# Performance work log

Hardware: AMD Instinct MI355X
Metric: run time of the kernel (lower is better)

The kernel has to match this reference:

```python
import jax, jax.numpy as jnp
import numpy as np

B, N, H_DIM = 64, 128, 128
NODE_S, NODE_V = 64, 32            # irreps_node = 64x0e + 32x1o -> dim 160
OUT_S, OUT_V = 32, 16              # out irreps  = 32x0e + 16x1o -> dim 80
RBF, ZEMB, HID, LAT, EDIM, NE = 16, 32, 128, 256, 16, 512
EATT = 4096
CUTOFF = 5.0
MAXZ = 100
NODE_DIM = NODE_S + 3 * NODE_V
OUT_DIM = OUT_S + 3 * OUT_V
WN = NODE_S*OUT_S + NODE_V*OUT_S + NODE_S*OUT_V + NODE_V*OUT_V  # 4608 TP weights per edge
GATE_IN = H_DIM + H_DIM + RBF + 1

def _lin(k, fi, fo):
    return jax.random.normal(k, (fi, fo), jnp.float32) / np.sqrt(fi)

def setup_inputs() -> dict:
    ks = jax.random.split(jax.random.key(0), 24)
    flat = B * N
    att_dist = jax.random.uniform(ks[0], (EATT,), jnp.float32, 0.05, CUTOFF)
    dirs = jax.random.normal(ks[1], (EATT, 3), jnp.float32)
    dirs = dirs / jnp.linalg.norm(dirs, axis=-1, keepdims=True)
    return dict(
        h=jax.random.normal(ks[2], (B, N, H_DIM), jnp.float32),
        h_full=jax.random.normal(ks[3], (B, N, NODE_DIM), jnp.float32),
        z=jax.random.randint(ks[4], (B, N), 1, MAXZ + 1),
        mask=jnp.ones((B, N), bool),
        e_feat=jax.random.normal(ks[5], (NE, EDIM), jnp.float32),
        absorber_index=jax.random.randint(ks[6], (B,), 0, N),
        att_dst=jax.random.randint(ks[7], (EATT,), 0, flat),
        att_dist=att_dist,
        att_vec=dirs * att_dist[:, None],
        w_zemb=jax.random.normal(ks[8], (MAXZ + 1, ZEMB), jnp.float32),
        w1_rad=_lin(ks[9], ZEMB + 1 + RBF, HID), b1_rad=jnp.zeros(HID, jnp.float32),
        w2_rad=_lin(ks[10], HID, WN), b2_rad=jnp.zeros(WN, jnp.float32),
        wg1=_lin(ks[11], GATE_IN, HID), bg1=jnp.zeros(HID, jnp.float32),
        wg2=_lin(ks[12], HID, 1), bg2=jnp.zeros(1, jnp.float32),
        we1=_lin(ks[13], EDIM, HID), be1=jnp.zeros(HID, jnp.float32),
        we2=_lin(ks[14], HID, OUT_S + OUT_V), be2=jnp.ones(OUT_S + OUT_V, jnp.float32),
        wo1=_lin(ks[15], OUT_S + OUT_V, HID), bo1=jnp.zeros(HID, jnp.float32),
        wo2=_lin(ks[16], HID, HID), bo2=jnp.zeros(HID, jnp.float32),
        wo3=_lin(ks[17], HID, LAT), bo3=jnp.zeros(LAT, jnp.float32),
    )

def _core(h, h_full, z, e_feat, absorber_index, att_dst, att_dist, att_vec,
          w_zemb, w1_rad, b1_rad, w2_rad, b2_rad, wg1, bg1, wg2, bg2,
          we1, be1, we2, be2, wo1, bo1, wo2, bo2, wo3, bo3):
    B_, N_, H_ = h.shape
    flat = B_ * N_
    dt = h.dtype
    # scatter edge data into flat (B*N) buffers
    amask = jnp.zeros((flat,), bool).at[att_dst].set(True)
    dflat = jnp.zeros((flat,), dt).at[att_dst].set(att_dist.astype(dt))
    vflat = jnp.zeros((flat, 3), dt).at[att_dst].set(att_vec.astype(dt))
    eps = jnp.maximum(dflat, 1e-8)
    u = vflat / eps[:, None]
    # component-normalized real spherical harmonics, lmax=1: Y0 = 1, Y1 = sqrt(3)*u
    ys = jnp.ones((flat, 1), dt)
    yv = jnp.sqrt(jnp.asarray(3.0, dt)) * u
    # Gaussian RBF on distance
    centers = jnp.linspace(0.0, CUTOFF, RBF).astype(dt)
    width = CUTOFF / (RBF - 1)
    rbf = jnp.exp(-0.5 * ((dflat[:, None] - centers) / width) ** 2)
    zr = w_zemb[z].reshape(flat, ZEMB)
    is_abs = jax.nn.one_hot(absorber_index, N_, dtype=dt)  # (B,N)
    win = jnp.concatenate([zr, is_abs.reshape(flat, 1), rbf], -1)
    tpw = jax.nn.silu(win @ w1_rad + b1_rad) @ w2_rad + b2_rad  # (flat, WN)
    o = 0
    wA = tpw[:, o:o + NODE_S*OUT_S].reshape(flat, NODE_S, OUT_S); o += NODE_S*OUT_S
    wB = tpw[:, o:o + NODE_V*OUT_S].reshape(flat, NODE_V, OUT_S); o += NODE_V*OUT_S
    wC = tpw[:, o:o + NODE_S*OUT_V].reshape(flat, NODE_S, OUT_V); o += NODE_S*OUT_V
    wD = tpw[:, o:o + NODE_V*OUT_V].reshape(flat, NODE_V, OUT_V)
    hf = h_full.reshape(flat, NODE_DIM)
    s1 = hf[:, :NODE_S]
    v1 = hf[:, NODE_S:].reshape(flat, NODE_V, 3)
    norm = 1.0 / np.sqrt(NODE_S + NODE_V)   # TP path (fan-in) normalization
    inv_s3 = 1.0 / np.sqrt(3.0)             # CG(1,1->0) = delta/sqrt(3)
    out_s = (jnp.einsum('ei,eio->eo', s1 * ys, wA)
             + jnp.einsum('eic,ec,eio->eo', v1, yv, wB) * inv_s3) * norm
    out_v = (jnp.einsum('ei,eio->eo', s1, wC)[:, :, None] * yv[:, None, :]
             + jnp.einsum('eic,eio->eoc', v1, wD) * ys[:, :, None]) * norm
    ve = jnp.concatenate([out_s, out_v.reshape(flat, 3 * OUT_V)], -1)
    env = jnp.where(dflat < CUTOFF, 0.5 * (jnp.cos(np.pi * dflat / CUTOFF) + 1.0), 0.0)[:, None]
    ve = ve * env
    # PaiNN-style scalar edge gate
    h_abs = jnp.take_along_axis(h, absorber_index[:, None, None], axis=1)  # (B,1,H)
    gate_in = jnp.concatenate([jnp.broadcast_to(h_abs, (B_, N_, H_)), h,
                               rbf.reshape(B_, N_, RBF), is_abs[..., None]], -1)
    gate = jax.nn.sigmoid(jax.nn.silu(gate_in @ wg1 + bg1) @ wg2 + bg2).reshape(flat, 1)
    ve = ve * gate * amask[:, None].astype(dt)
    v_abs = ve.reshape(B_, N_, OUT_DIM).sum(1)  # (B, OUT_DIM)
    # energy irrep modulation: per-mul scalar from energy features
    scales = jax.nn.silu(e_feat @ we1 + be1) @ we2 + be2  # (nE, OUT_S+OUT_V)
    scale_full = jnp.concatenate([scales[:, :OUT_S], jnp.repeat(scales[:, OUT_S:], 3, axis=-1)], -1)
    v_mod = v_abs[:, None, :] * scale_full[None]  # (B, nE, OUT_DIM)
    vecs = v_mod[..., OUT_S:].reshape(B_, scales.shape[0], OUT_V, 3)
    inv = jnp.concatenate([v_mod[..., :OUT_S], jnp.sqrt(jnp.sum(vecs * vecs, -1) + 1e-12)], -1)
    x = jax.nn.silu(inv @ wo1 + bo1)
    x = jax.nn.silu(x @ wo2 + bo2)
    return x @ wo3 + bo3  # (B, nE, LAT)

def reference(h, h_full, z, mask, e_feat, absorber_index, att_dst, att_dist, att_vec,
              w_zemb, w1_rad, b1_rad, w2_rad, b2_rad, wg1, bg1, wg2, bg2,
              we1, be1, we2, be2, wo1, bo1, wo2, bo2, wo3, bo3):
    # mask is computed into att_mask in the original but never used downstream
    return _core(h, h_full, z, e_feat, absorber_index, att_dst, att_dist, att_vec,
                 w_zemb, w1_rad, b1_rad, w2_rad, b2_rad, wg1, bg1, wg2, bg2,
                 we1, be1, we2, be2, wo1, bo1, wo2, bo2, wo3, bo3)
```

## Files before the change

### kernel.cpp

```cpp
#include <hip/hip_runtime.h>
#include <math.h>

#define FLAT   8192
#define NB     64
#define OD_    80
#define NE_    512
#define EATT_  4096
#define MAXACT 4096
#define PARTW 1088

typedef __bf16 v8bf __attribute__((ext_vector_type(8)));
typedef float  v4f  __attribute__((ext_vector_type(4)));

__device__ __forceinline__ float silu_f(float x) { return x / (1.f + __expf(-x)); }
__device__ __forceinline__ float sigm_f(float x) { return 1.f / (1.f + __expf(-x)); }

__device__ __forceinline__ void transpose_split(const float* __restrict__ src, int ld,
                                                int nbase, __bf16* wh, __bf16* wl,
                                                float (*lds)[129]) {
  int t = threadIdx.x;
#pragma unroll
  for (int it = 0; it < 16; ++it) {
    int idx = it * 256 + t;
    int r = idx >> 5, c4 = idx & 31;
    float4 v = *(const float4*)(src + (size_t)r * ld + nbase + c4 * 4);
    lds[r][c4 * 4 + 0] = v.x;
    lds[r][c4 * 4 + 1] = v.y;
    lds[r][c4 * 4 + 2] = v.z;
    lds[r][c4 * 4 + 3] = v.w;
  }
  __syncthreads();
  int n = t >> 1, kh = (t & 1) * 64;
  union { __bf16 b[64]; uint4 u[8]; } H, L;
#pragma unroll
  for (int k = 0; k < 64; ++k) {
    float v = lds[kh + k][n];
    __bf16 hv = (__bf16)v;
    H.b[k] = hv;
    L.b[k] = (__bf16)(v - (float)hv);
  }
  uint4* ph = (uint4*)(wh + (size_t)(nbase + n) * 128 + kh);
  uint4* pl = (uint4*)(wl + (size_t)(nbase + n) * 128 + kh);
#pragma unroll
  for (int i = 0; i < 8; ++i) { ph[i] = H.u[i]; pl[i] = L.u[i]; }
}

__global__ __launch_bounds__(256) void k_prep(
    const float* __restrict__ w2_rad, const float* __restrict__ wo2,
    const float* __restrict__ wo3,
    const int* __restrict__ abs_idx, const float* __restrict__ h,
    const float* __restrict__ wg1,
    __bf16* w2rt_h, __bf16* w2rt_l, __bf16* w2t_h, __bf16* w2t_l,
    __bf16* w3t_h, __bf16* w3t_l,
    float* habs_g, float* vabs, int* widx, int* count) {
  __shared__ float lds[128][129];
  int bid = blockIdx.x;
  int t = threadIdx.x;
  if (bid < 36) {
    transpose_split(w2_rad, 4608, bid * 128, w2rt_h, w2rt_l, lds);
  } else if (bid < 37) {
    transpose_split(wo2, 128, 0, w2t_h, w2t_l, lds);
  } else if (bid < 39) {
    transpose_split(wo3, 256, (bid - 37) * 128, w3t_h, w3t_l, lds);
  } else if (bid < 71) {
    float* hs = &lds[0][0];
    int half = t >> 7, tt = t & 127;
    int b = (bid - 39) * 2 + half;
    int nabs = abs_idx[b];
    hs[half * 128 + tt] = h[(size_t)(b * 128 + nabs) * 128 + tt];
    __syncthreads();
    float g = 0.f;
    for (int c = 0; c < 128; ++c) g = fmaf(hs[half * 128 + c], wg1[c * 128 + tt], g);
    habs_g[b * 128 + tt] = g;
  } else {
    int g = (bid - 71) * 256 + t;
    if (g < FLAT) widx[g] = -1;
    if (g < NB * OD_) vabs[g] = 0.f;
    if (g == 0) *count = 0;
  }
}

__global__ void k_scatter(const int* __restrict__ att_dst, int* widx) {
  int i = blockIdx.x * 256 + threadIdx.x;
  if (i < EATT_) atomicMax(&widx[att_dst[i]], i);
}

__global__ void k_build(const int* __restrict__ widx, int* active, int* count) {
  int j = blockIdx.x * 256 + threadIdx.x;
  if (j < FLAT && widx[j] >= 0) {
    int p = atomicAdd(count, 1);
    active[p] = j;
  }
}

__global__ __launch_bounds__(128) void k_node4(
    const int* __restrict__ count, const int* __restrict__ active,
    const int* __restrict__ widx,
    const float* __restrict__ att_dist, const float* __restrict__ att_vec,
    const int* __restrict__ z, const float* __restrict__ w_zemb,
    const int* __restrict__ abs_idx,
    const float* __restrict__ w1_rad, const float* __restrict__ b1_rad,
    const float* __restrict__ h, const float* __restrict__ habs_g,
    const float* __restrict__ wg1, const float* __restrict__ bg1,
    const float* __restrict__ wg2, const float* __restrict__ bg2,
    const float* __restrict__ h_full,
    __bf16* ah_glob, __bf16* al_glob,
    float* coef_glob, float* meta_f, int* meta_b) {
  int cnt = *count;
  int pbase = blockIdx.x * 4;
  if (pbase >= cnt) return;
  int t = threadIdx.x;

  __shared__ float win[4][49];
  __shared__ float yv_s[4][3];
  __shared__ float sh_d[4];
  __shared__ float red[4][128];
  __shared__ float hsh[4][128];

  bool ok[4];
  int jj[4], ee[4], bb[4];
  float isab[4];
#pragma unroll
  for (int q = 0; q < 4; ++q) {
    int pos = pbase + q;
    ok[q] = pos < cnt;
    jj[q] = ok[q] ? active[pos] : 0;
    ee[q] = ok[q] ? widx[jj[q]] : 0;
    if (ee[q] < 0) ee[q] = 0;
    bb[q] = jj[q] >> 7;
    isab[q] = ((jj[q] & 127) == abs_idx[bb[q]]) ? 1.f : 0.f;
  }

  if (t < 4) {
    int q = t;
    float d = att_dist[ee[q]];
    sh_d[q] = d;
    float eps = fmaxf(d, 1e-8f);
    const float s3 = 1.7320508075688772f;
    yv_s[q][0] = s3 * att_vec[ee[q] * 3 + 0] / eps;
    yv_s[q][1] = s3 * att_vec[ee[q] * 3 + 1] / eps;
    yv_s[q][2] = s3 * att_vec[ee[q] * 3 + 2] / eps;
  }
#pragma unroll
  for (int q = 0; q < 4; ++q) {
    if (t < 32) win[q][t] = w_zemb[z[jj[q]] * 32 + t];
    if (t == 32) win[q][32] = isab[q];
    if (t >= 33 && t < 49) {
      int k = t - 33;
      float d = att_dist[ee[q]];
      float x = (d - (float)k * (1.f / 3.f)) * 3.f;
      win[q][t] = __expf(-0.5f * x * x);
    }
    hsh[q][t] = h[(size_t)jj[q] * 128 + t];
  }
  __syncthreads();

  {
    float s[4];
    float bv = b1_rad[t];
#pragma unroll
    for (int q = 0; q < 4; ++q) s[q] = bv;
    for (int k = 0; k < 49; ++k) {
      float wv = w1_rad[k * 128 + t];
#pragma unroll
      for (int q = 0; q < 4; ++q) s[q] = fmaf(win[q][k], wv, s[q]);
    }
#pragma unroll
    for (int q = 0; q < 4; ++q) {
      if (ok[q]) {
        float av = silu_f(s[q]);
        __bf16 hv = (__bf16)av;
        ah_glob[(size_t)(pbase + q) * 128 + t] = hv;
        al_glob[(size_t)(pbase + q) * 128 + t] = (__bf16)(av - (float)hv);
      }
    }
  }

  {
    float g[4];
#pragma unroll
    for (int q = 0; q < 4; ++q) g[q] = bg1[t] + habs_g[bb[q] * 128 + t];
    for (int c = 0; c < 128; ++c) {
      float wv = wg1[(128 + c) * 128 + t];
#pragma unroll
      for (int q = 0; q < 4; ++q) g[q] = fmaf(hsh[q][c], wv, g[q]);
    }
    for (int k = 0; k < 16; ++k) {
      float wv = wg1[(256 + k) * 128 + t];
#pragma unroll
      for (int q = 0; q < 4; ++q) g[q] = fmaf(win[q][33 + k], wv, g[q]);
    }
    {
      float wv = wg1[272 * 128 + t];
#pragma unroll
      for (int q = 0; q < 4; ++q) g[q] = fmaf(isab[q], wv, g[q]);
    }
    float w2v = wg2[t];
#pragma unroll
    for (int q = 0; q < 4; ++q) red[q][t] = silu_f(g[q]) * w2v;
  }
  __syncthreads();

#pragma unroll
  for (int q = 0; q < 4; ++q) {
    if (!ok[q]) continue;
    int pos = pbase + q;
    const float* hf = h_full + (size_t)jj[q] * 160;
    if (t < 64) coef_glob[pos * 192 + t] = hf[t];
    if (t >= 64 && t < 96) {
      int i = t - 64;
      float pv = hf[64 + i * 3 + 0] * yv_s[q][0] + hf[64 + i * 3 + 1] * yv_s[q][1] +
                 hf[64 + i * 3 + 2] * yv_s[q][2];
      coef_glob[pos * 192 + t] = pv * 0.5773502691896258f;
    }
    if (t < 96) coef_glob[pos * 192 + 96 + t] = hf[64 + t];
  }

  if (t < 4) {
    int q = t;
    if (ok[q]) {
      int pos = pbase + q;
      float tot = 0.f;
      for (int k = 0; k < 128; ++k) tot += red[q][k];
      tot += bg2[0];
      float gate = sigm_f(tot);
      float d = sh_d[q];
      float env = (d < 5.f) ? 0.5f * (__cosf(3.14159265358979323846f * d * 0.2f) + 1.f) : 0.f;
      meta_f[pos * 4 + 0] = yv_s[q][0];
      meta_f[pos * 4 + 1] = yv_s[q][1];
      meta_f[pos * 4 + 2] = yv_s[q][2];
      meta_f[pos * 4 + 3] = gate * env;
      meta_b[pos] = bb[q];
    }
  }
}

__global__ __launch_bounds__(256) void k_mrgemm(
    const int* __restrict__ count,
    const __bf16* Ah, const __bf16* Al,
    const __bf16* __restrict__ Bh, const __bf16* __restrict__ Bl,
    const float* __restrict__ b2, const float* __restrict__ coef_glob,
    float* __restrict__ part) {
  int cc = blockIdx.x;
  int nbase = blockIdx.y * 128;
  int cnt = *count;
  if (nbase >= cnt) return;
  int t = threadIdx.x;
  int w = t >> 6, l = t & 63;
  int kg = l >> 4, ln = l & 15;
  int cbase = cc * 128;

  __shared__ v8bf Bs[2][2][8][64];

  size_t brow0 = (size_t)(cbase + w * 16 + ln) * 128 + kg * 8;
  size_t brow1 = (size_t)(cbase + (w + 4) * 16 + ln) * 128 + kg * 8;
  size_t arow0 = (size_t)(nbase + (2 * w) * 16 + ln) * 128 + kg * 8;
  size_t arow1 = (size_t)(nbase + (2 * w + 1) * 16 + ln) * 128 + kg * 8;

  v8bf rb0 = *(const v8bf*)(Bh + brow0);
  v8bf rb1 = *(const v8bf*)(Bh + brow1);
  v8bf rb2 = *(const v8bf*)(Bl + brow0);
  v8bf rb3 = *(const v8bf*)(Bl + brow1);
  v8bf ah0 = *(const v8bf*)(Ah + arow0);
  v8bf al0 = *(const v8bf*)(Al + arow0);
  v8bf ah1 = *(const v8bf*)(Ah + arow1);
  v8bf al1 = *(const v8bf*)(Al + arow1);
  Bs[0][0][w][l]     = rb0;
  Bs[0][0][w + 4][l] = rb1;
  Bs[0][1][w][l]     = rb2;
  Bs[0][1][w + 4][l] = rb3;
  __syncthreads();

  v4f acc[2][8];
  v4f z4 = {0.f, 0.f, 0.f, 0.f};
#pragma unroll
  for (int i = 0; i < 2; ++i)
#pragma unroll
    for (int j = 0; j < 8; ++j) acc[i][j] = z4;

  for (int kb = 0; kb < 4; ++kb) {
    int cur = kb & 1;
    v8bf nb0, nb1, nb2, nb3, nh0, nl0, nh1, nl1;
    if (kb < 3) {
      int off = (kb + 1) * 32;
      nb0 = *(const v8bf*)(Bh + brow0 + off);
      nb1 = *(const v8bf*)(Bh + brow1 + off);
      nb2 = *(const v8bf*)(Bl + brow0 + off);
      nb3 = *(const v8bf*)(Bl + brow1 + off);
      nh0 = *(const v8bf*)(Ah + arow0 + off);
      nl0 = *(const v8bf*)(Al + arow0 + off);
      nh1 = *(const v8bf*)(Ah + arow1 + off);
      nl1 = *(const v8bf*)(Al + arow1 + off);
    }
#pragma unroll
    for (int nt = 0; nt < 8; ++nt) {
      v8bf bh = Bs[cur][0][nt][l];
      v8bf bl = Bs[cur][1][nt][l];
      acc[0][nt] = __builtin_amdgcn_mfma_f32_16x16x32_bf16(ah0, bh, acc[0][nt], 0, 0, 0);
      acc[0][nt] = __builtin_amdgcn_mfma_f32_16x16x32_bf16(al0, bh, acc[0][nt], 0, 0, 0);
      acc[0][nt] = __builtin_amdgcn_mfma_f32_16x16x32_bf16(ah0, bl, acc[0][nt], 0, 0, 0);
      acc[1][nt] = __builtin_amdgcn_mfma_f32_16x16x32_bf16(ah1, bh, acc[1][nt], 0, 0, 0);
      acc[1][nt] = __builtin_amdgcn_mfma_f32_16x16x32_bf16(al1, bh, acc[1][nt], 0, 0, 0);
      acc[1][nt] = __builtin_amdgcn_mfma_f32_16x16x32_bf16(ah1, bl, acc[1][nt], 0, 0, 0);
    }
    if (kb < 3) {
      int nxt = cur ^ 1;
      Bs[nxt][0][w][l]     = nb0;
      Bs[nxt][0][w + 4][l] = nb1;
      Bs[nxt][1][w][l]     = nb2;
      Bs[nxt][1][w + 4][l] = nb3;
      ah0 = nh0; al0 = nl0; ah1 = nh1; al1 = nl1;
    }
    __syncthreads();
  }

  float b2v[8];
#pragma unroll
  for (int nt = 0; nt < 8; ++nt) b2v[nt] = b2[cbase + nt * 16 + ln];

#pragma unroll
  for (int mi = 0; mi < 2; ++mi) {
    int nodeb = nbase + (2 * w + mi) * 16 + kg * 4;
#pragma unroll
    for (int j = 0; j < 4; ++j) {
      int nd = nodeb + j;
      if (nd >= cnt) continue;
      const float* cf = coef_glob + (size_t)nd * 192;
      if (cc < 24) {
        float s0 = 0.f, s1 = 0.f;
#pragma unroll
        for (int m = 0; m < 4; ++m) {
          float c = cf[cc * 4 + m];
          s0 = fmaf(acc[mi][2 * m][j] + b2v[2 * m], c, s0);
          s1 = fmaf(acc[mi][2 * m + 1][j] + b2v[2 * m + 1], c, s1);
        }
        float* pp = part + (size_t)nd * PARTW + cc * 32 + ln;
        pp[0]  = s0;
        pp[16] = s1;
      } else if (cc < 32) {
        float s = 0.f;
#pragma unroll
        for (int nt = 0; nt < 8; ++nt)
          s = fmaf(acc[mi][nt][j] + b2v[nt], cf[(cc - 24) * 8 + nt], s);
        part[(size_t)nd * PARTW + 768 + (cc - 24) * 16 + ln] = s;
      } else {
        float s0 = 0.f, s1 = 0.f, s2 = 0.f;
#pragma unroll
        for (int nt = 0; nt < 8; ++nt) {
          float x = acc[mi][nt][j] + b2v[nt];
          const float* c3 = cf + 96 + ((cc - 32) * 8 + nt) * 3;
          s0 = fmaf(x, c3[0], s0);
          s1 = fmaf(x, c3[1], s1);
          s2 = fmaf(x, c3[2], s2);
        }
        float* pp = part + (size_t)nd * PARTW + 896 + (cc - 32) * 48 + ln;
        pp[0]  = s0;
        pp[16] = s1;
        pp[32] = s2;
      }
    }
  }
}

__global__ __launch_bounds__(256) void k_post(
    const int* __restrict__ count, const float* __restrict__ part,
    const float* __restrict__ meta_f, const int* __restrict__ meta_b, float* vabs,
    const float* __restrict__ e_feat,
    const float* __restrict__ we1, const float* __restrict__ be1,
    const float* __restrict__ we2, const float* __restrict__ be2, float* sfull) {
  __shared__ float hid[128];
  int t = threadIdx.x;
  if (blockIdx.x < 2048) {
    int pos = blockIdx.x * 2 + (t >> 7);
    int slot = t & 127;
    if (pos >= *count || slot >= 96) return;
    const float* pp = part + (size_t)pos * PARTW;
    float s = 0.f;
    if (slot < 32) {
#pragma unroll
      for (int c = 0; c < 24; ++c) s += pp[c * 32 + slot];
    } else if (slot < 48) {
#pragma unroll
      for (int c = 0; c < 8; ++c) s += pp[768 + c * 16 + (slot - 32)];
    } else {
#pragma unroll
      for (int c = 0; c < 4; ++c) s += pp[896 + c * 48 + (slot - 48)];
    }
    float sc = meta_f[pos * 4 + 3] * 0.10206207261596577f;
    float* vb = vabs + meta_b[pos] * 80;
    if (slot < 32) {
      unsafeAtomicAdd(&vb[slot], s * sc);
    } else if (slot < 48) {
      int o = slot - 32;
      float q = s * sc;
      unsafeAtomicAdd(&vb[32 + o * 3 + 0], q * meta_f[pos * 4 + 0]);
      unsafeAtomicAdd(&vb[32 + o * 3 + 1], q * meta_f[pos * 4 + 1]);
      unsafeAtomicAdd(&vb[32 + o * 3 + 2], q * meta_f[pos * 4 + 2]);
    } else {
      int s2 = slot - 48;
      int comp = s2 >> 4, o = s2 & 15;
      unsafeAtomicAdd(&vb[32 + o * 3 + comp], s * sc);
    }
  } else {
    int row = blockIdx.x - 2048;
    if (t < 128) {
      const float* ef = e_feat + row * 16;
      float s = be1[t];
      for (int k = 0; k < 16; ++k) s = fmaf(ef[k], we1[k * 128 + t], s);
      hid[t] = silu_f(s);
    }
    __syncthreads();
    if (t < 48) {
      float o = be2[t];
      for (int k = 0; k < 128; ++k) o = fmaf(hid[k], we2[k * 48 + t], o);
      if (t < 32) sfull[row * 80 + t] = o;
      else {
        int oo = t - 32;
        sfull[row * 80 + 32 + oo * 3 + 0] = o;
        sfull[row * 80 + 32 + oo * 3 + 1] = o;
        sfull[row * 80 + 32 + oo * 3 + 2] = o;
      }
    }
  }
}

__global__ __launch_bounds__(256) void k_hg1(const float* __restrict__ vabs,
                                             const float* __restrict__ sfull,
                                             const float* __restrict__ wo1,
                                             const float* __restrict__ bo1,
                                             __bf16* __restrict__ xh,
                                             __bf16* __restrict__ xl) {
  int rbase = blockIdx.x * 64;
  int b = rbase >> 9;
  int e0 = rbase & 511;
  int t = threadIdx.x;
  int tx = t & 15, ty = t >> 4;
  int n0 = ty * 4;

  __shared__ float w_s[48 * 128];
  __shared__ float invt[48][64];
  __shared__ float va[80];

  if (t < 80) va[t] = vabs[b * 80 + t];
  {
    const float4* wg = (const float4*)wo1;
    float4* ws4 = (float4*)w_s;
#pragma unroll
    for (int it = 0; it < 6; ++it) ws4[t + it * 256] = wg[t + it * 256];
  }
  __syncthreads();

  for (int idx = t; idx < 48 * 64; idx += 256) {
    int cd = idx >> 6, r = idx & 63;
    const float* sf = sfull + (size_t)(e0 + r) * 80;
    float v;
    if (cd < 32) v = va[cd] * sf[cd];
    else {
      int base = 32 + (cd - 32) * 3;
      float m0 = va[base + 0] * sf[base + 0];
      float m1 = va[base + 1] * sf[base + 1];
      float m2 = va[base + 2] * sf[base + 2];
      v = sqrtf(m0 * m0 + m1 * m1 + m2 * m2 + 1e-12f);
    }
    invt[cd][r] = v;
  }
  __syncthreads();

  float acc[4][8];
#pragma unroll
  for (int i = 0; i < 4; ++i)
#pragma unroll
    for (int j = 0; j < 8; ++j) acc[i][j] = 0.f;

  for (int k = 0; k < 48; ++k) {
    float4 av  = *(const float4*)&invt[k][n0];
    float4 w0  = *(const float4*)&w_s[k * 128 + tx * 4];
    float4 w1v = *(const float4*)&w_s[k * 128 + 64 + tx * 4];
#pragma unroll
    for (int i = 0; i < 4; ++i) {
      float a = (i == 0) ? av.x : (i == 1) ? av.y : (i == 2) ? av.z : av.w;
      acc[i][0] = fmaf(a, w0.x,  acc[i][0]);
      acc[i][1] = fmaf(a, w0.y,  acc[i][1]);
      acc[i][2] = fmaf(a, w0.z,  acc[i][2]);
      acc[i][3] = fmaf(a, w0.w,  acc[i][3]);
      acc[i][4] = fmaf(a, w1v.x, acc[i][4]);
      acc[i][5] = fmaf(a, w1v.y, acc[i][5]);
      acc[i][6] = fmaf(a, w1v.z, acc[i][6]);
      acc[i][7] = fmaf(a, w1v.w, acc[i][7]);
    }
  }

  float4 bq0 = *(const float4*)(bo1 + tx * 4);
  float4 bq1 = *(const float4*)(bo1 + 64 + tx * 4);
#pragma unroll
  for (int i = 0; i < 4; ++i) {
    size_t row = (size_t)(rbase + n0 + i);
    float q0[4] = {silu_f(acc[i][0] + bq0.x), silu_f(acc[i][1] + bq0.y),
                   silu_f(acc[i][2] + bq0.z), silu_f(acc[i][3] + bq0.w)};
    float q1[4] = {silu_f(acc[i][4] + bq1.x), silu_f(acc[i][5] + bq1.y),
                   silu_f(acc[i][6] + bq1.z), silu_f(acc[i][7] + bq1.w)};
    union { __bf16 bb[4]; uint2 u; } H, L;
#pragma unroll
    for (int e = 0; e < 4; ++e) {
      __bf16 hv = (__bf16)q0[e];
      H.bb[e] = hv;
      L.bb[e] = (__bf16)(q0[e] - (float)hv);
    }
    *(uint2*)(xh + row * 128 + tx * 4) = H.u;
    *(uint2*)(xl + row * 128 + tx * 4) = L.u;
#pragma unroll
    for (int e = 0; e < 4; ++e) {
      __bf16 hv = (__bf16)q1[e];
      H.bb[e] = hv;
      L.bb[e] = (__bf16)(q1[e] - (float)hv);
    }
    *(uint2*)(xh + row * 128 + 64 + tx * 4) = H.u;
    *(uint2*)(xl + row * 128 + 64 + tx * 4) = L.u;
  }
}

template<int MODE>
__global__ __launch_bounds__(256) void k_mgemm(
    const __bf16* Ah, const __bf16* Al,
    const __bf16* __restrict__ Bh, const __bf16* __restrict__ Bl,
    const float* __restrict__ bias,
    __bf16* Oh, __bf16* Ol, float* __restrict__ Of) {
  int rbase = blockIdx.y * 64;
  int cbase = blockIdx.x * 128;
  int t = threadIdx.x;
  int w = t >> 6;
  int l = t & 63;
  int kg = l >> 4, ln = l & 15;

  __shared__ v8bf As[2][2][4][64];
  __shared__ v8bf Bs[2][2][8][64];

  size_t arow  = (size_t)(rbase + w * 16 + ln) * 128 + kg * 8;
  int nt0 = w, nt1 = w + 4;
  size_t brow0 = (size_t)(cbase + nt0 * 16 + ln) * 128 + kg * 8;
  size_t brow1 = (size_t)(cbase + nt1 * 16 + ln) * 128 + kg * 8;

  v8bf ra0, ra1, rb0, rb1, rb2, rb3;
  ra0 = *(const v8bf*)(Ah + arow);
  ra1 = *(const v8bf*)(Al + arow);
  rb0 = *(const v8bf*)(Bh + brow0);
  rb1 = *(const v8bf*)(Bh + brow1);
  rb2 = *(const v8bf*)(Bl + brow0);
  rb3 = *(const v8bf*)(Bl + brow1);
  As[0][0][w][l]   = ra0;
  As[0][1][w][l]   = ra1;
  Bs[0][0][nt0][l] = rb0;
  Bs[0][0][nt1][l] = rb1;
  Bs[0][1][nt0][l] = rb2;
  Bs[0][1][nt1][l] = rb3;
  __syncthreads();

  v4f acc[8];
  v4f z4 = {0.f, 0.f, 0.f, 0.f};
#pragma unroll
  for (int i = 0; i < 8; ++i) acc[i] = z4;

  for (int kb = 0; kb < 4; ++kb) {
    int cur = kb & 1;
    if (kb < 3) {
      int off = (kb + 1) * 32;
      ra0 = *(const v8bf*)(Ah + arow + off);
      ra1 = *(const v8bf*)(Al + arow + off);
      rb0 = *(const v8bf*)(Bh + brow0 + off);
      rb1 = *(const v8bf*)(Bh + brow1 + off);
      rb2 = *(const v8bf*)(Bl + brow0 + off);
      rb3 = *(const v8bf*)(Bl + brow1 + off);
    }
    v8bf ah  = As[cur][0][w][l];
    v8bf alo = As[cur][1][w][l];
#pragma unroll
    for (int nt = 0; nt < 8; ++nt) {
      v8bf bh = Bs[cur][0][nt][l];
      v8bf bl = Bs[cur][1][nt][l];
      acc[nt] = __builtin_amdgcn_mfma_f32_16x16x32_bf16(ah,  bh, acc[nt], 0, 0, 0);
      acc[nt] = __builtin_amdgcn_mfma_f32_16x16x32_bf16(alo, bh, acc[nt], 0, 0, 0);
      acc[nt] = __builtin_amdgcn_mfma_f32_16x16x32_bf16(ah,  bl, acc[nt], 0, 0, 0);
    }
    if (kb < 3) {
      int nxt = cur ^ 1;
      As[nxt][0][w][l]   = ra0;
      As[nxt][1][w][l]   = ra1;
      Bs[nxt][0][nt0][l] = rb0;
      Bs[nxt][0][nt1][l] = rb1;
      Bs[nxt][1][nt0][l] = rb2;
      Bs[nxt][1][nt1][l] = rb3;
    }
    __syncthreads();
  }

  int r0 = rbase + w * 16 + kg * 4;
#pragma unroll
  for (int nt = 0; nt < 8; ++nt) {
    float bv = bias[cbase + nt * 16 + ln];
#pragma unroll
    for (int j = 0; j < 4; ++j) {
      float x = acc[nt][j] + bv;
      if (MODE == 0) {
        x = silu_f(x);
        __bf16 hv = (__bf16)x;
        size_t o = (size_t)(r0 + j) * 128 + nt * 16 + ln;
        Oh[o] = hv;
        Ol[o] = (__bf16)(x - (float)hv);
      } else {
        Of[(size_t)(r0 + j) * 256 + cbase + nt * 16 + ln] = x;
      }
    }
  }
}

extern "C" void kernel_launch(void* const* d_in, const int* in_sizes, int n_in,
                              void* d_out, int out_size, void* d_ws, size_t ws_size,
                              hipStream_t stream) {
  const float* h        = (const float*)d_in[0];
  const float* h_full   = (const float*)d_in[1];
  const int*   z        = (const int*)d_in[2];
  const float* e_feat   = (const float*)d_in[4];
  const int*   abs_idx  = (const int*)d_in[5];
  const int*   att_dst  = (const int*)d_in[6];
  const float* att_dist = (const float*)d_in[7];
  const float* att_vec  = (const float*)d_in[8];
  const float* w_zemb   = (const float*)d_in[9];
  const float* w1_rad   = (const float*)d_in[10];
  const float* b1_rad   = (const float*)d_in[11];
  const float* w2_rad   = (const float*)d_in[12];
  const float* b2_rad   = (const float*)d_in[13];
  const float* wg1      = (const float*)d_in[14];
  const float* bg1      = (const float*)d_in[15];
  const float* wg2      = (const float*)d_in[16];
  const float* bg2      = (const float*)d_in[17];
  const float* we1      = (const float*)d_in[18];
  const float* be1      = (const float*)d_in[19];
  const float* we2      = (const float*)d_in[20];
  const float* be2      = (const float*)d_in[21];
  const float* wo1      = (const float*)d_in[22];
  const float* bo1      = (const float*)d_in[23];
  const float* wo2      = (const float*)d_in[24];
  const float* bo2      = (const float*)d_in[25];
  const float* wo3      = (const float*)d_in[26];
  const float* bo3      = (const float*)d_in[27];
  float* out = (float*)d_out;

  float* meta_f  = (float*)d_ws;
  float* vabs    = meta_f + MAXACT * 4;
  float* sfull   = vabs + NB * OD_;
  float* habs_g  = sfull + NE_ * OD_;
  __bf16* w2t_h  = (__bf16*)(habs_g + NB * 128);
  __bf16* w2t_l  = w2t_h + 128 * 128;
  __bf16* w3t_h  = w2t_l + 128 * 128;
  __bf16* w3t_l  = w3t_h + 256 * 128;
  int* widx   = (int*)(w3t_l + 256 * 128);
  int* active = widx + FLAT;
  int* meta_b = active + MAXACT;
  int* count  = meta_b + MAXACT;
  float* big  = (float*)(count + 15);
  __bf16* ah_glob  = (__bf16*)big;
  __bf16* al_glob  = ah_glob + MAXACT * 128;
  float* coef_glob = (float*)(al_glob + MAXACT * 128);
  __bf16* w2rt_h   = (__bf16*)(coef_glob + MAXACT * 192);
  __bf16* w2rt_l   = w2rt_h + 4608 * 128;
  float* part      = (float*)(w2rt_l + 4608 * 128);
  __bf16* xh       = (__bf16*)big;
  __bf16* xl       = xh + (size_t)32768 * 128;

  k_prep<<<103, 256, 0, stream>>>(w2_rad, wo2, wo3, abs_idx, h, wg1,
                                  w2rt_h, w2rt_l, w2t_h, w2t_l, w3t_h, w3t_l,
                                  habs_g, vabs, widx, count);
  k_scatter<<<16, 256, 0, stream>>>(att_dst, widx);
  k_build<<<32, 256, 0, stream>>>(widx, active, count);
  k_node4<<<1024, 128, 0, stream>>>(count, active, widx, att_dist, att_vec, z, w_zemb,
                                    abs_idx, w1_rad, b1_rad, h, habs_g, wg1, bg1, wg2, bg2,
                                    h_full, ah_glob, al_glob, coef_glob, meta_f, meta_b);
  k_mrgemm<<<dim3(36, 32), 256, 0, stream>>>(count, ah_glob, al_glob, w2rt_h, w2rt_l,
                                             b2_rad, coef_glob, part);
  k_post<<<2560, 256, 0, stream>>>(count, part, meta_f, meta_b, vabs,
                                   e_feat, we1, be1, we2, be2, sfull);
  k_hg1<<<512, 256, 0, stream>>>(vabs, sfull, wo1, bo1, xh, xl);
  k_mgemm<0><<<dim3(1, 512), 256, 0, stream>>>(xh, xl, w2t_h, w2t_l, bo2,
                                               xh, xl, nullptr);
  k_mgemm<1><<<dim3(2, 512), 256, 0, stream>>>(xh, xl, w3t_h, w3t_l, bo3,
                                               nullptr, nullptr, out);
}
```

Before: 234.5 us.

## Fuse output MLP head into one kernel and reduce TP partials in GEMM

The three output MLP stages (wo1 layer, wo2 MFMA GEMM, wo3 MFMA GEMM) are merged into a single k_head kernel that keeps intermediate activations in LDS instead of round-tripping bf16 hi/lo buffers through global memory. The radial-weight GEMM now has each block process three column chunks and accumulate the coefficient contractions in registers, so the partial buffer shrinks and the combine step sums fewer partials. The energy-scale MLP moves into the prep kernel. The trade-off is fewer blocks for the radial GEMM (lower parallelism) and heavy LDS use per block in the fused head, which may limit occupancy.

After: 454.6 us. 1.94x slower.

```diff
diff --git a/kernel.cpp b/kernel.cpp
--- a/kernel.cpp
+++ b/kernel.cpp
@@ -7,7 +7,7 @@
 #define NE_    512
 #define EATT_  4096
 #define MAXACT 4096
-#define PARTW 1088
+#define PARTW2 400
 
 typedef __bf16 v8bf __attribute__((ext_vector_type(8)));
 typedef float  v4f  __attribute__((ext_vector_type(4)));
@@ -50,9 +50,12 @@
     const float* __restrict__ wo3,
     const int* __restrict__ abs_idx, const float* __restrict__ h,
     const float* __restrict__ wg1,
+    const float* __restrict__ e_feat,
+    const float* __restrict__ we1, const float* __restrict__ be1,
+    const float* __restrict__ we2, const float* __restrict__ be2,
     __bf16* w2rt_h, __bf16* w2rt_l, __bf16* w2t_h, __bf16* w2t_l,
     __bf16* w3t_h, __bf16* w3t_l,
-    float* habs_g, float* vabs, int* widx, int* count) {
+    float* habs_g, float* vabs, int* widx, int* count, float* sfull) {
   __shared__ float lds[128][129];
   int bid = blockIdx.x;
   int t = threadIdx.x;
@@ -72,11 +75,31 @@
     float g = 0.f;
     for (int c = 0; c < 128; ++c) g = fmaf(hs[half * 128 + c], wg1[c * 128 + tt], g);
     habs_g[b * 128 + tt] = g;
-  } else {
+  } else if (bid < 103) {
     int g = (bid - 71) * 256 + t;
     if (g < FLAT) widx[g] = -1;
     if (g < NB * OD_) vabs[g] = 0.f;
     if (g == 0) *count = 0;
+  } else {
+    float* hid = &lds[0][0];
+    int half = t >> 7, tt = t & 127;
+    int row = (bid - 103) * 2 + half;
+    const float* ef = e_feat + row * 16;
+    float s = be1[tt];
+    for (int k = 0; k < 16; ++k) s = fmaf(ef[k], we1[k * 128 + tt], s);
+    hid[half * 128 + tt] = silu_f(s);
+    __syncthreads();
+    if (tt < 48) {
+      float o = be2[tt];
+      for (int k = 0; k < 128; ++k) o = fmaf(hid[half * 128 + k], we2[k * 48 + tt], o);
+      if (tt < 32) sfull[row * 80 + tt] = o;
+      else {
+        int oo = tt - 32;
+        sfull[row * 80 + 32 + oo * 3 + 0] = o;
+        sfull[row * 80 + 32 + oo * 3 + 1] = o;
+        sfull[row * 80 + 32 + oo * 3 + 2] = o;
+      }
+    }
   }
 }
 
@@ -235,40 +258,45 @@
   }
 }
 
-__global__ __launch_bounds__(256) void k_mrgemm(
+__global__ __launch_bounds__(256) void k_mrgemm2(
     const int* __restrict__ count,
-    const __bf16* Ah, const __bf16* Al,
+    const __bf16* __restrict__ Ah, const __bf16* __restrict__ Al,
     const __bf16* __restrict__ Bh, const __bf16* __restrict__ Bl,
     const float* __restrict__ b2, const float* __restrict__ coef_glob,
-    float* __restrict__ part) {
-  int cc = blockIdx.x;
+    float* __restrict__ part2) {
+  int g = blockIdx.x;
   int nbase = blockIdx.y * 128;
   int cnt = *count;
   if (nbase >= cnt) return;
   int t = threadIdx.x;
   int w = t >> 6, l = t & 63;
   int kg = l >> 4, ln = l & 15;
-  int cbase = cc * 128;
 
   __shared__ v8bf Bs[2][2][8][64];
 
-  size_t brow0 = (size_t)(cbase + w * 16 + ln) * 128 + kg * 8;
-  size_t brow1 = (size_t)(cbase + (w + 4) * 16 + ln) * 128 + kg * 8;
-  size_t arow0 = (size_t)(nbase + (2 * w) * 16 + ln) * 128 + kg * 8;
-  size_t arow1 = (size_t)(nbase + (2 * w + 1) * 16 + ln) * 128 + kg * 8;
-
-  v8bf rb0 = *(const v8bf*)(Bh + brow0);
-  v8bf rb1 = *(const v8bf*)(Bh + brow1);
-  v8bf rb2 = *(const v8bf*)(Bl + brow0);
-  v8bf rb3 = *(const v8bf*)(Bl + brow1);
-  v8bf ah0 = *(const v8bf*)(Ah + arow0);
-  v8bf al0 = *(const v8bf*)(Al + arow0);
-  v8bf ah1 = *(const v8bf*)(Ah + arow1);
-  v8bf al1 = *(const v8bf*)(Al + arow1);
-  Bs[0][0][w][l]     = rb0;
-  Bs[0][0][w + 4][l] = rb1;
-  Bs[0][1][w][l]     = rb2;
-  Bs[0][1][w + 4][l] = rb3;
+  v8bf Afh[2][4], Afl[2][4];
+#pragma unroll
+  for (int mi = 0; mi < 2; ++mi) {
+    size_t ar = (size_t)(nbase + (2 * w + mi) * 16 + ln) * 128 + kg * 8;
+#pragma unroll
+    for (int kb = 0; kb < 4; ++kb) {
+      Afh[mi][kb] = *(const v8bf*)(Ah + ar + kb * 32);
+      Afl[mi][kb] = *(const v8bf*)(Al + ar + kb * 32);
+    }
+  }
+
+  float sS0[2][4] = {}, sS1[2][4] = {}, sQ[2][4] = {};
+  float sD[2][4][3] = {};
+
+  {
+    int cc0 = g * 3;
+    size_t p0 = (size_t)(cc0 * 128 + w * 16 + ln) * 128 + kg * 8;
+    size_t p1 = (size_t)(cc0 * 128 + (w + 4) * 16 + ln) * 128 + kg * 8;
+    Bs[0][0][w][l]     = *(const v8bf*)(Bh + p0);
+    Bs[0][0][w + 4][l] = *(const v8bf*)(Bh + p1);
+    Bs[0][1][w][l]     = *(const v8bf*)(Bl + p0);
+    Bs[0][1][w + 4][l] = *(const v8bf*)(Bl + p1);
+  }
   __syncthreads();
 
   v4f acc[2][8];
@@ -278,336 +306,400 @@
 #pragma unroll
     for (int j = 0; j < 8; ++j) acc[i][j] = z4;
 
-  for (int kb = 0; kb < 4; ++kb) {
-    int cur = kb & 1;
-    v8bf nb0, nb1, nb2, nb3, nh0, nl0, nh1, nl1;
-    if (kb < 3) {
-      int off = (kb + 1) * 32;
-      nb0 = *(const v8bf*)(Bh + brow0 + off);
-      nb1 = *(const v8bf*)(Bh + brow1 + off);
-      nb2 = *(const v8bf*)(Bl + brow0 + off);
-      nb3 = *(const v8bf*)(Bl + brow1 + off);
-      nh0 = *(const v8bf*)(Ah + arow0 + off);
-      nl0 = *(const v8bf*)(Al + arow0 + off);
-      nh1 = *(const v8bf*)(Ah + arow1 + off);
-      nl1 = *(const v8bf*)(Al + arow1 + off);
+  for (int s = 0; s < 12; ++s) {
+    int cur = s & 1;
+    int kb = s & 3, ci = s >> 2;
+    v8bf r0, r1, r2, r3;
+    if (s < 11) {
+      int cc_n = g * 3 + ((s + 1) >> 2), kb_n = (s + 1) & 3;
+      size_t p0 = (size_t)(cc_n * 128 + w * 16 + ln) * 128 + kb_n * 32 + kg * 8;
+      size_t p1 = (size_t)(cc_n * 128 + (w + 4) * 16 + ln) * 128 + kb_n * 32 + kg * 8;
+      r0 = *(const v8bf*)(Bh + p0);
+      r1 = *(const v8bf*)(Bh + p1);
+      r2 = *(const v8bf*)(Bl + p0);
+      r3 = *(const v8bf*)(Bl + p1);
     }
 #pragma unroll
     for (int nt = 0; nt < 8; ++nt) {
       v8bf bh = Bs[cur][0][nt][l];
       v8bf bl = Bs[cur][1][nt][l];
-      acc[0][nt] = __builtin_amdgcn_mfma_f32_16x16x32_bf16(ah0, bh, acc[0][nt], 0, 0, 0);
-      acc[0][nt] = __builtin_amdgcn_mfma_f32_16x16x32_bf16(al0, bh, acc[0][nt], 0, 0, 0);
-      acc[0][nt] = __builtin_amdgcn_mfma_f32_16x16x32_bf16(ah0, bl, acc[0][nt], 0, 0, 0);
-      acc[1][nt] = __builtin_amdgcn_mfma_f32_16x16x32_bf16(ah1, bh, acc[1][nt], 0, 0, 0);
-      acc[1][nt] = __builtin_amdgcn_mfma_f32_16x16x32_bf16(al1, bh, acc[1][nt], 0, 0, 0);
-      acc[1][nt] = __builtin_amdgcn_mfma_f32_16x16x32_bf16(ah1, bl, acc[1][nt], 0, 0, 0);
-    }
-    if (kb < 3) {
+      acc[0][nt] = __builtin_amdgcn_mfma_f32_16x16x32_bf16(Afh[0][kb], bh, acc[0][nt], 0, 0, 0);
+      acc[0][nt] = __builtin_amdgcn_mfma_f32_16x16x32_bf16(Afl[0][kb], bh, acc[0][nt], 0, 0, 0);
+      acc[0][nt] = __builtin_amdgcn_mfma_f32_16x16x32_bf16(Afh[0][kb], bl, acc[0][nt], 0, 0, 0);
+      acc[1][nt] = __builtin_amdgcn_mfma_f32_16x16x32_bf16(Afh[1][kb], bh, acc[1][nt], 0, 0, 0);
+      acc[1][nt] = __builtin_amdgcn_mfma_f32_16x16x32_bf16(Afl[1][kb], bh, acc[1][nt], 0, 0, 0);
+      acc[1][nt] = __builtin_amdgcn_mfma_f32_16x16x32_bf16(Afh[1][kb], bl, acc[1][nt], 0, 0, 0);
+    }
+    if (s < 11) {
       int nxt = cur ^ 1;
-      Bs[nxt][0][w][l]     = nb0;
-      Bs[nxt][0][w + 4][l] = nb1;
-      Bs[nxt][1][w][l]     = nb2;
-      Bs[nxt][1][w + 4][l] = nb3;
-      ah0 = nh0; al0 = nl0; ah1 = nh1; al1 = nl1;
+      Bs[nxt][0][w][l]     = r0;
+      Bs[nxt][0][w + 4][l] = r1;
+      Bs[nxt][1][w][l]     = r2;
+      Bs[nxt][1][w + 4][l] = r3;
     }
     __syncthreads();
-  }
-
-  float b2v[8];
-#pragma unroll
-  for (int nt = 0; nt < 8; ++nt) b2v[nt] = b2[cbase + nt * 16 + ln];
+
+    if (kb == 3) {
+      int cc = g * 3 + ci;
+      float b2v[8];
+#pragma unroll
+      for (int nt = 0; nt < 8; ++nt) b2v[nt] = b2[cc * 128 + nt * 16 + ln];
+#pragma unroll
+      for (int mi = 0; mi < 2; ++mi) {
+        int nodeb = nbase + (2 * w + mi) * 16 + kg * 4;
+#pragma unroll
+        for (int j = 0; j < 4; ++j) {
+          int nd = nodeb + j;
+          if (nd >= cnt) continue;
+          const float* cf = coef_glob + (size_t)nd * 192;
+          if (cc < 24) {
+            float s0 = 0.f, s1 = 0.f;
+#pragma unroll
+            for (int m = 0; m < 4; ++m) {
+              float c = cf[cc * 4 + m];
+              s0 = fmaf(acc[mi][2 * m][j] + b2v[2 * m], c, s0);
+              s1 = fmaf(acc[mi][2 * m + 1][j] + b2v[2 * m + 1], c, s1);
+            }
+            sS0[mi][j] += s0;
+            sS1[mi][j] += s1;
+          } else if (cc < 32) {
+            float sq = 0.f;
+#pragma unroll
+            for (int nt = 0; nt < 8; ++nt)
+              sq = fmaf(acc[mi][nt][j] + b2v[nt], cf[(cc - 24) * 8 + nt], sq);
+            sQ[mi][j] += sq;
+          } else {
+            float s0 = 0.f, s1 = 0.f, s2 = 0.f;
+#pragma unroll
+            for (int nt = 0; nt < 8; ++nt) {
+              float x = acc[mi][nt][j] + b2v[nt];
+              const float* c3 = cf + 96 + ((cc - 32) * 8 + nt) * 3;
+              s0 = fmaf(x, c3[0], s0);
+              s1 = fmaf(x, c3[1], s1);
+              s2 = fmaf(x, c3[2], s2);
+            }
+            sD[mi][j][0] += s0;
+            sD[mi][j][1] += s1;
+            sD[mi][j][2] += s2;
+          }
+        }
+      }
+#pragma unroll
+      for (int i = 0; i < 2; ++i)
+#pragma unroll
+        for (int j = 0; j < 8; ++j) acc[i][j] = z4;
+    }
+  }
 
 #pragma unroll
   for (int mi = 0; mi < 2; ++mi) {
-    int nodeb = nbase + (2 * w + mi) * 16 + kg * 4;
 #pragma unroll
     for (int j = 0; j < 4; ++j) {
-      int nd = nodeb + j;
+      int nd = nbase + (2 * w + mi) * 16 + kg * 4 + j;
       if (nd >= cnt) continue;
-      const float* cf = coef_glob + (size_t)nd * 192;
-      if (cc < 24) {
-        float s0 = 0.f, s1 = 0.f;
-#pragma unroll
-        for (int m = 0; m < 4; ++m) {
-          float c = cf[cc * 4 + m];
-          s0 = fmaf(acc[mi][2 * m][j] + b2v[2 * m], c, s0);
-          s1 = fmaf(acc[mi][2 * m + 1][j] + b2v[2 * m + 1], c, s1);
-        }
-        float* pp = part + (size_t)nd * PARTW + cc * 32 + ln;
-        pp[0]  = s0;
-        pp[16] = s1;
-      } else if (cc < 32) {
-        float s = 0.f;
-#pragma unroll
-        for (int nt = 0; nt < 8; ++nt)
-          s = fmaf(acc[mi][nt][j] + b2v[nt], cf[(cc - 24) * 8 + nt], s);
-        part[(size_t)nd * PARTW + 768 + (cc - 24) * 16 + ln] = s;
+      float* pw = part2 + (size_t)nd * PARTW2;
+      if (g < 8) {
+        pw[g * 32 + ln]      = sS0[mi][j];
+        pw[g * 32 + 16 + ln] = sS1[mi][j];
+      } else if (g < 10) {
+        pw[256 + (g - 8) * 16 + ln] = sQ[mi][j];
+      } else if (g == 10) {
+        pw[256 + 2 * 16 + ln] = sQ[mi][j];
+        pw[304 + ln]      = sD[mi][j][0];
+        pw[304 + 16 + ln] = sD[mi][j][1];
+        pw[304 + 32 + ln] = sD[mi][j][2];
       } else {
-        float s0 = 0.f, s1 = 0.f, s2 = 0.f;
-#pragma unroll
-        for (int nt = 0; nt < 8; ++nt) {
-          float x = acc[mi][nt][j] + b2v[nt];
-          const float* c3 = cf + 96 + ((cc - 32) * 8 + nt) * 3;
-          s0 = fmaf(x, c3[0], s0);
-          s1 = fmaf(x, c3[1], s1);
-          s2 = fmaf(x, c3[2], s2);
-        }
-        float* pp = part + (size_t)nd * PARTW + 896 + (cc - 32) * 48 + ln;
-        pp[0]  = s0;
-        pp[16] = s1;
-        pp[32] = s2;
-      }
-    }
-  }
-}
-
-__global__ __launch_bounds__(256) void k_post(
-    const int* __restrict__ count, const float* __restrict__ part,
-    const float* __restrict__ meta_f, const int* __restrict__ meta_b, float* vabs,
-    const float* __restrict__ e_feat,
-    const float* __restrict__ we1, const float* __restrict__ be1,
-    const float* __restrict__ we2, const float* __restrict__ be2, float* sfull) {
-  __shared__ float hid[128];
+        pw[304 + 48 + ln]      = sD[mi][j][0];
+        pw[304 + 48 + 16 + ln] = sD[mi][j][1];
+        pw[304 + 48 + 32 + ln] = sD[mi][j][2];
+      }
+    }
+  }
+}
+
+__global__ void k_combine(const int* __restrict__ count, const float* __restrict__ part2,
+                          const float* __restrict__ meta_f, const int* __restrict__ meta_b,
+                          float* vabs) {
   int t = threadIdx.x;
-  if (blockIdx.x < 2048) {
-    int pos = blockIdx.x * 2 + (t >> 7);
-    int slot = t & 127;
-    if (pos >= *count || slot >= 96) return;
-    const float* pp = part + (size_t)pos * PARTW;
-    float s = 0.f;
-    if (slot < 32) {
-#pragma unroll
-      for (int c = 0; c < 24; ++c) s += pp[c * 32 + slot];
-    } else if (slot < 48) {
-#pragma unroll
-      for (int c = 0; c < 8; ++c) s += pp[768 + c * 16 + (slot - 32)];
-    } else {
-#pragma unroll
-      for (int c = 0; c < 4; ++c) s += pp[896 + c * 48 + (slot - 48)];
-    }
-    float sc = meta_f[pos * 4 + 3] * 0.10206207261596577f;
-    float* vb = vabs + meta_b[pos] * 80;
-    if (slot < 32) {
-      unsafeAtomicAdd(&vb[slot], s * sc);
-    } else if (slot < 48) {
-      int o = slot - 32;
-      float q = s * sc;
-      unsafeAtomicAdd(&vb[32 + o * 3 + 0], q * meta_f[pos * 4 + 0]);
-      unsafeAtomicAdd(&vb[32 + o * 3 + 1], q * meta_f[pos * 4 + 1]);
-      unsafeAtomicAdd(&vb[32 + o * 3 + 2], q * meta_f[pos * 4 + 2]);
-    } else {
-      int s2 = slot - 48;
-      int comp = s2 >> 4, o = s2 & 15;
-      unsafeAtomicAdd(&vb[32 + o * 3 + comp], s * sc);
-    }
+  int pos = blockIdx.x * 2 + (t >> 7);
+  int slot = t & 127;
+  if (pos >= *count || slot >= 96) return;
+  const float* pp = part2 + (size_t)pos * PARTW2;
+  float s = 0.f;
+  if (slot < 32) {
+#pragma unroll
+    for (int c = 0; c < 8; ++c) s += pp[c * 32 + slot];
+  } else if (slot < 48) {
+#pragma unroll
+    for (int c = 0; c < 3; ++c) s += pp[256 + c * 16 + (slot - 32)];
   } else {
-    int row = blockIdx.x - 2048;
-    if (t < 128) {
-      const float* ef = e_feat + row * 16;
-      float s = be1[t];
-      for (int k = 0; k < 16; ++k) s = fmaf(ef[k], we1[k * 128 + t], s);
-      hid[t] = silu_f(s);
-    }
-    __syncthreads();
-    if (t < 48) {
-      float o = be2[t];
-      for (int k = 0; k < 128; ++k) o = fmaf(hid[k], we2[k * 48 + t], o);
-      if (t < 32) sfull[row * 80 + t] = o;
-      else {
-        int oo = t - 32;
-        sfull[row * 80 + 32 + oo * 3 + 0] = o;
-        sfull[row * 80 + 32 + oo * 3 + 1] = o;
-        sfull[row * 80 + 32 + oo * 3 + 2] = o;
-      }
-    }
-  }
-}
-
-__global__ __launch_bounds__(256) void k_hg1(const float* __restrict__ vabs,
-                                             const float* __restrict__ sfull,
-                                             const float* __restrict__ wo1,
-                                             const float* __restrict__ bo1,
-                                             __bf16* __restrict__ xh,
-                                             __bf16* __restrict__ xl) {
+#pragma unroll
+    for (int c = 0; c < 2; ++c) s += pp[304 + c * 48 + (slot - 48)];
+  }
+  float sc = meta_f[pos * 4 + 3] * 0.10206207261596577f;
+  float* vb = vabs + meta_b[pos] * 80;
+  if (slot < 32) {
+    unsafeAtomicAdd(&vb[slot], s * sc);
+  } else if (slot < 48) {
+    int o = slot - 32;
+    float q = s * sc;
+    unsafeAtomicAdd(&vb[32 + o * 3 + 0], q * meta_f[pos * 4 + 0]);
+    unsafeAtomicAdd(&vb[32 + o * 3 + 1], q * meta_f[pos * 4 + 1]);
+    unsafeAtomicAdd(&vb[32 + o * 3 + 2], q * meta_f[pos * 4 + 2]);
+  } else {
+    int s2 = slot - 48;
+    int comp = s2 >> 4, o = s2 & 15;
+    unsafeAtomicAdd(&vb[32 + o * 3 + comp], s * sc);
+  }
+}
+
+__global__ __launch_bounds__(256) void k_head(
+    const float* __restrict__ vabs, const float* __restrict__ sfull,
+    const float* __restrict__ wo1, const float* __restrict__ bo1,
+    const __bf16* __restrict__ W2h, const __bf16* __restrict__ W2l,
+    const float* __restrict__ bo2,
+    const __bf16* __restrict__ W3h, const __bf16* __restrict__ W3l,
+    const float* __restrict__ bo3,
+    float* __restrict__ out) {
+  __shared__ __align__(16) char arena[69632];
+  float* w_s = (float*)arena;
+  float (*invt)[64] = (float(*)[64])(arena + 24576);
+  float* va = (float*)(arena + 36864);
+  char* xsh = arena;
+  char* xsl = arena + 16384;
+  v8bf (*BsB)[2][8][64] = (v8bf(*)[2][8][64])(arena + 36864);
+  char* ysh = arena + 36864;
+  char* ysl = arena + 53248;
+  v8bf (*BsC)[2][8][64] = (v8bf(*)[2][8][64])arena;
+
   int rbase = blockIdx.x * 64;
   int b = rbase >> 9;
   int e0 = rbase & 511;
   int t = threadIdx.x;
-  int tx = t & 15, ty = t >> 4;
-  int n0 = ty * 4;
-
-  __shared__ float w_s[48 * 128];
-  __shared__ float invt[48][64];
-  __shared__ float va[80];
-
-  if (t < 80) va[t] = vabs[b * 80 + t];
+
   {
-    const float4* wg = (const float4*)wo1;
-    float4* ws4 = (float4*)w_s;
-#pragma unroll
-    for (int it = 0; it < 6; ++it) ws4[t + it * 256] = wg[t + it * 256];
+    int tx = t & 15, ty = t >> 4;
+    int n0 = ty * 4;
+    if (t < 80) va[t] = vabs[b * 80 + t];
+    {
+      const float4* wg = (const float4*)wo1;
+      float4* ws4 = (float4*)w_s;
+#pragma unroll
+      for (int it = 0; it < 6; ++it) ws4[t + it * 256] = wg[t + it * 256];
+    }
+    __syncthreads();
+
+    for (int idx = t; idx < 48 * 64; idx += 256) {
+      int cd = idx >> 6, r = idx & 63;
+      const float* sf = sfull + (size_t)(e0 + r) * 80;
+      float v;
+      if (cd < 32) v = va[cd] * sf[cd];
+      else {
+        int base = 32 + (cd - 32) * 3;
+        float m0 = va[base + 0] * sf[base + 0];
+        float m1 = va[base + 1] * sf[base + 1];
+        float m2 = va[base + 2] * sf[base + 2];
+        v = sqrtf(m0 * m0 + m1 * m1 + m2 * m2 + 1e-12f);
+      }
+      invt[cd][r] = v;
+    }
+    __syncthreads();
+
+    float acc[4][8];
+#pragma unroll
+    for (int i = 0; i < 4; ++i)
+#pragma unroll
+      for (int j = 0; j < 8; ++j) acc[i][j] = 0.f;
+
+    for (int k = 0; k < 48; ++k) {
+      float4 av  = *(const float4*)&invt[k][n0];
+      float4 w0  = *(const float4*)&w_s[k * 128 + tx * 4];
+      float4 w1v = *(const float4*)&w_s[k * 128 + 64 + tx * 4];
+#pragma unroll
+      for (int i = 0; i < 4; ++i) {
+        float a = (i == 0) ? av.x : (i == 1) ? av.y : (i == 2) ? av.z : av.w;
+        acc[i][0] = fmaf(a, w0.x,  acc[i][0]);
+        acc[i][1] = fmaf(a, w0.y,  acc[i][1]);
+        acc[i][2] = fmaf(a, w0.z,  acc[i][2]);
+        acc[i][3] = fmaf(a, w0.w,  acc[i][3]);
+        acc[i][4] = fmaf(a, w1v.x, acc[i][4]);
+        acc[i][5] = fmaf(a, w1v.y, acc[i][5]);
+        acc[i][6] = fmaf(a, w1v.z, acc[i][6]);
+        acc[i][7] = fmaf(a, w1v.w, acc[i][7]);
+      }
+    }
+    __syncthreads();
+
+    float4 bq0 = *(const float4*)(bo1 + tx * 4);
+    float4 bq1 = *(const float4*)(bo1 + 64 + tx * 4);
+#pragma unroll
+    for (int i = 0; i < 4; ++i) {
+      int row = n0 + i;
+      int sw = (row & 7) << 4;
+      float q0[4] = {silu_f(acc[i][0] + bq0.x), silu_f(acc[i][1] + bq0.y),
+                     silu_f(acc[i][2] + bq0.z), silu_f(acc[i][3] + bq0.w)};
+      float q1[4] = {silu_f(acc[i][4] + bq1.x), silu_f(acc[i][5] + bq1.y),
+                     silu_f(acc[i][6] + bq1.z), silu_f(acc[i][7] + bq1.w)};
+      union { __bf16 bb[4]; uint2 u; } H, L;
+#pragma unroll
+      for (int e = 0; e < 4; ++e) {
+        __bf16 hv = (__bf16)q0[e];
+        H.bb[e] = hv;
+        L.bb[e] = (__bf16)(q0[e] - (float)hv);
+      }
+      *(uint2*)(xsh + ((row * 256 + tx * 8) ^ sw)) = H.u;
+      *(uint2*)(xsl + ((row * 256 + tx * 8) ^ sw)) = L.u;
+#pragma unroll
+      for (int e = 0; e < 4; ++e) {
+        __bf16 hv = (__bf16)q1[e];
+        H.bb[e] = hv;
+        L.bb[e] = (__bf16)(q1[e] - (float)hv);
+      }
+      *(uint2*)(xsh + ((row * 256 + 128 + tx * 8) ^ sw)) = H.u;
+      *(uint2*)(xsl + ((row * 256 + 128 + tx * 8) ^ sw)) = L.u;
+    }
   }
   __syncthreads();
 
-  for (int idx = t; idx < 48 * 64; idx += 256) {
-    int cd = idx >> 6, r = idx & 63;
-    const float* sf = sfull + (size_t)(e0 + r) * 80;
-    float v;
-    if (cd < 32) v = va[cd] * sf[cd];
-    else {
-      int base = 32 + (cd - 32) * 3;
-      float m0 = va[base + 0] * sf[base + 0];
-      float m1 = va[base + 1] * sf[base + 1];
-      float m2 = va[base + 2] * sf[base + 2];
-      v = sqrtf(m0 * m0 + m1 * m1 + m2 * m2 + 1e-12f);
-    }
-    invt[cd][r] = v;
+  int w = t >> 6, l = t & 63;
+  int kg = l >> 4, ln = l & 15;
+  {
+    int arw = w * 16 + ln;
+    int sw = (arw & 7) << 4;
+    v8bf axh[4], axl[4];
+#pragma unroll
+    for (int kb = 0; kb < 4; ++kb) {
+      int byt = arw * 256 + kb * 64 + kg * 16;
+      axh[kb] = *(v8bf*)(xsh + (byt ^ sw));
+      axl[kb] = *(v8bf*)(xsl + (byt ^ sw));
+    }
+    {
+      size_t p0 = (size_t)(w * 16 + ln) * 128 + kg * 8;
+      size_t p1 = (size_t)((w + 4) * 16 + ln) * 128 + kg * 8;
+      BsB[0][0][w][l]     = *(const v8bf*)(W2h + p0);
+      BsB[0][0][w + 4][l] = *(const v8bf*)(W2h + p1);
+      BsB[0][1][w][l]     = *(const v8bf*)(W2l + p0);
+      BsB[0][1][w + 4][l] = *(const v8bf*)(W2l + p1);
+    }
+    __syncthreads();
+
+    v4f acc[8];
+    v4f z4 = {0.f, 0.f, 0.f, 0.f};
+#pragma unroll
+    for (int i = 0; i < 8; ++i) acc[i] = z4;
+
+    for (int kb = 0; kb < 4; ++kb) {
+      int cur = kb & 1;
+      v8bf r0, r1, r2, r3;
+      if (kb < 3) {
+        size_t p0 = (size_t)(w * 16 + ln) * 128 + (kb + 1) * 32 + kg * 8;
+        size_t p1 = (size_t)((w + 4) * 16 + ln) * 128 + (kb + 1) * 32 + kg * 8;
+        r0 = *(const v8bf*)(W2h + p0);
+        r1 = *(const v8bf*)(W2h + p1);
+        r2 = *(const v8bf*)(W2l + p0);
+        r3 = *(const v8bf*)(W2l + p1);
+      }
+#pragma unroll
+      for (int nt = 0; nt < 8; ++nt) {
+        v8bf bh = BsB[cur][0][nt][l];
+        v8bf bl = BsB[cur][1][nt][l];
+        acc[nt] = __builtin_amdgcn_mfma_f32_16x16x32_bf16(axh[kb], bh, acc[nt], 0, 0, 0);
+        acc[nt] = __builtin_amdgcn_mfma_f32_16x16x32_bf16(axl[kb], bh, acc[nt], 0, 0, 0);
+        acc[nt] = __builtin_amdgcn_mfma_f32_16x16x32_bf16(axh[kb], bl, acc[nt], 0, 0, 0);
+      }
+      if (kb < 3) {
+        int nxt = cur ^ 1;
+        BsB[nxt][0][w][l]     = r0;
+        BsB[nxt][0][w + 4][l] = r1;
+        BsB[nxt][1][w][l]     = r2;
+        BsB[nxt][1][w + 4][l] = r3;
+      }
+      __syncthreads();
+    }
+
+    int r0l = w * 16 + kg * 4;
+#pragma unroll
+    for (int nt = 0; nt < 8; ++nt) {
+      float bv = bo2[nt * 16 + ln];
+#pragma unroll
+      for (int j = 0; j < 4; ++j) {
+        float x = silu_f(acc[nt][j] + bv);
+        int row = r0l + j;
+        int byt = (row * 256 + (nt * 16 + ln) * 2) ^ ((row & 7) << 4);
+        __bf16 hv = (__bf16)x;
+        *(__bf16*)(ysh + byt) = hv;
+        *(__bf16*)(ysl + byt) = (__bf16)(x - (float)hv);
+      }
+    }
   }
   __syncthreads();
 
-  float acc[4][8];
-#pragma unroll
-  for (int i = 0; i < 4; ++i)
-#pragma unroll
-    for (int j = 0; j < 8; ++j) acc[i][j] = 0.f;
-
-  for (int k = 0; k < 48; ++k) {
-    float4 av  = *(const float4*)&invt[k][n0];
-    float4 w0  = *(const float4*)&w_s[k * 128 + tx * 4];
-    float4 w1v = *(const float4*)&w_s[k * 128 + 64 + tx * 4];
-#pragma unroll
-    for (int i = 0; i < 4; ++i) {
-      float a = (i == 0) ? av.x : (i == 1) ? av.y : (i == 2) ? av.z : av.w;
-      acc[i][0] = fmaf(a, w0.x,  acc[i][0]);
-      acc[i][1] = fmaf(a, w0.y,  acc[i][1]);
-      acc[i][2] = fmaf(a, w0.z,  acc[i][2]);
-      acc[i][3] = fmaf(a, w0.w,  acc[i][3]);
-      acc[i][4] = fmaf(a, w1v.x, acc[i][4]);
-      acc[i][5] = fmaf(a, w1v.y, acc[i][5]);
-      acc[i][6] = fmaf(a, w1v.z, acc[i][6]);
-      acc[i][7] = fmaf(a, w1v.w, acc[i][7]);
-    }
-  }
-
-  float4 bq0 = *(const float4*)(bo1 + tx * 4);
-  float4 bq1 = *(const float4*)(bo1 + 64 + tx * 4);
-#pragma unroll
-  for (int i = 0; i < 4; ++i) {
-    size_t row = (size_t)(rbase + n0 + i);
-    float q0[4] = {silu_f(acc[i][0] + bq0.x), silu_f(acc[i][1] + bq0.y),
-                   silu_f(acc[i][2] + bq0.z), silu_f(acc[i][3] + bq0.w)};
-    float q1[4] = {silu_f(acc[i][4] + bq1.x), silu_f(acc[i][5] + bq1.y),
-                   silu_f(acc[i][6] + bq1.z), silu_f(acc[i][7] + bq1.w)};
-    union { __bf16 bb[4]; uint2 u; } H, L;
-#pragma unroll
-    for (int e = 0; e < 4; ++e) {
-      __bf16 hv = (__bf16)q0[e];
-      H.bb[e] = hv;
-      L.bb[e] = (__bf16)(q0[e] - (float)hv);
-    }
-    *(uint2*)(xh + row * 128 + tx * 4) = H.u;
-    *(uint2*)(xl + row * 128 + tx * 4) = L.u;
-#pragma unroll
-    for (int e = 0; e < 4; ++e) {
-      __bf16 hv = (__bf16)q1[e];
-      H.bb[e] = hv;
-      L.bb[e] = (__bf16)(q1[e] - (float)hv);
-    }
-    *(uint2*)(xh + row * 128 + 64 + tx * 4) = H.u;
-    *(uint2*)(xl + row * 128 + 64 + tx * 4) = L.u;
-  }
-}
-
-template<int MODE>
-__global__ __launch_bounds__(256) void k_mgemm(
-    const __bf16* Ah, const __bf16* Al,
-    const __bf16* __restrict__ Bh, const __bf16* __restrict__ Bl,
-    const float* __restrict__ bias,
-    __bf16* Oh, __bf16* Ol, float* __restrict__ Of) {
-  int rbase = blockIdx.y * 64;
-  int cbase = blockIdx.x * 128;
-  int t = threadIdx.x;
-  int w = t >> 6;
-  int l = t & 63;
-  int kg = l >> 4, ln = l & 15;
-
-  __shared__ v8bf As[2][2][4][64];
-  __shared__ v8bf Bs[2][2][8][64];
-
-  size_t arow  = (size_t)(rbase + w * 16 + ln) * 128 + kg * 8;
-  int nt0 = w, nt1 = w + 4;
-  size_t brow0 = (size_t)(cbase + nt0 * 16 + ln) * 128 + kg * 8;
-  size_t brow1 = (size_t)(cbase + nt1 * 16 + ln) * 128 + kg * 8;
-
-  v8bf ra0, ra1, rb0, rb1, rb2, rb3;
-  ra0 = *(const v8bf*)(Ah + arow);
-  ra1 = *(const v8bf*)(Al + arow);
-  rb0 = *(const v8bf*)(Bh + brow0);
-  rb1 = *(const v8bf*)(Bh + brow1);
-  rb2 = *(const v8bf*)(Bl + brow0);
-  rb3 = *(const v8bf*)(Bl + brow1);
-  As[0][0][w][l]   = ra0;
-  As[0][1][w][l]   = ra1;
-  Bs[0][0][nt0][l] = rb0;
-  Bs[0][0][nt1][l] = rb1;
-  Bs[0][1][nt0][l] = rb2;
-  Bs[0][1][nt1][l] = rb3;
-  __syncthreads();
-
-  v4f acc[8];
-  v4f z4 = {0.f, 0.f, 0.f, 0.f};
-#pragma unroll
-  for (int i = 0; i < 8; ++i) acc[i] = z4;
-
-  for (int kb = 0; kb < 4; ++kb) {
-    int cur = kb & 1;
-    if (kb < 3) {
-      int off = (kb + 1) * 32;
-      ra0 = *(const v8bf*)(Ah + arow + off);
-      ra1 = *(const v8bf*)(Al + arow + off);
-      rb0 = *(const v8bf*)(Bh + brow0 + off);
-      rb1 = *(const v8bf*)(Bh + brow1 + off);
-      rb2 = *(const v8bf*)(Bl + brow0 + off);
-      rb3 = *(const v8bf*)(Bl + brow1 + off);
-    }
-    v8bf ah  = As[cur][0][w][l];
-    v8bf alo = As[cur][1][w][l];
-#pragma unroll
-    for (int nt = 0; nt < 8; ++nt) {
-      v8bf bh = Bs[cur][0][nt][l];
-      v8bf bl = Bs[cur][1][nt][l];
-      acc[nt] = __builtin_amdgcn_mfma_f32_16x16x32_bf16(ah,  bh, acc[nt], 0, 0, 0);
-      acc[nt] = __builtin_amdgcn_mfma_f32_16x16x32_bf16(alo, bh, acc[nt], 0, 0, 0);
-      acc[nt] = __builtin_amdgcn_mfma_f32_16x16x32_bf16(ah,  bl, acc[nt], 0, 0, 0);
-    }
-    if (kb < 3) {
-      int nxt = cur ^ 1;
-      As[nxt][0][w][l]   = ra0;
-      As[nxt][1][w][l]   = ra1;
-      Bs[nxt][0][nt0][l] = rb0;
-      Bs[nxt][0][nt1][l] = rb1;
-      Bs[nxt][1][nt0][l] = rb2;
-      Bs[nxt][1][nt1][l] = rb3;
+  {
+    int arw = w * 16 + ln;
+    int sw = (arw & 7) << 4;
+    v8bf ayh[4], ayl[4];
+#pragma unroll
+    for (int kb = 0; kb < 4; ++kb) {
+      int byt = arw * 256 + kb * 64 + kg * 16;
+      ayh[kb] = *(v8bf*)(ysh + (byt ^ sw));
+      ayl[kb] = *(v8bf*)(ysl + (byt ^ sw));
     }
     __syncthreads();
-  }
-
-  int r0 = rbase + w * 16 + kg * 4;
-#pragma unroll
-  for (int nt = 0; nt < 8; ++nt) {
-    float bv = bias[cbase + nt * 16 + ln];
-#pragma unroll
-    for (int j = 0; j < 4; ++j) {
-      float x = acc[nt][j] + bv;
-      if (MODE == 0) {
-        x = silu_f(x);
-        __bf16 hv = (__bf16)x;
-        size_t o = (size_t)(r0 + j) * 128 + nt * 16 + ln;
-        Oh[o] = hv;
-        Ol[o] = (__bf16)(x - (float)hv);
-      } else {
-        Of[(size_t)(r0 + j) * 256 + cbase + nt * 16 + ln] = x;
+
+    for (int ch = 0; ch < 2; ++ch) {
+      int cbase = ch * 128;
+      {
+        size_t p0 = (size_t)(cbase + w * 16 + ln) * 128 + kg * 8;
+        size_t p1 = (size_t)(cbase + (w + 4) * 16 + ln) * 128 + kg * 8;
+        BsC[0][0][w][l]     = *(const v8bf*)(W3h + p0);
+        BsC[0][0][w + 4][l] = *(const v8bf*)(W3h + p1);
+        BsC[0][1][w][l]     = *(const v8bf*)(W3l + p0);
+        BsC[0][1][w + 4][l] = *(const v8bf*)(W3l + p1);
+      }
+      __syncthreads();
+
+      v4f acc[8];
+      v4f z4 = {0.f, 0.f, 0.f, 0.f};
+#pragma unroll
+      for (int i = 0; i < 8; ++i) acc[i] = z4;
+
+      for (int kb = 0; kb < 4; ++kb) {
+        int cur = kb & 1;
+        v8bf r0, r1, r2, r3;
+        if (kb < 3) {
+          size_t p0 = (size_t)(cbase + w * 16 + ln) * 128 + (kb + 1) * 32 + kg * 8;
+          size_t p1 = (size_t)(cbase + (w + 4) * 16 + ln) * 128 + (kb + 1) * 32 + kg * 8;
+          r0 = *(const v8bf*)(W3h + p0);
+          r1 = *(const v8bf*)(W3h + p1);
+          r2 = *(const v8bf*)(W3l + p0);
+          r3 = *(const v8bf*)(W3l + p1);
+        }
+#pragma unroll
+        for (int nt = 0; nt < 8; ++nt) {
+          v8bf bh = BsC[cur][0][nt][l];
+          v8bf bl = BsC[cur][1][nt][l];
+          acc[nt] = __builtin_amdgcn_mfma_f32_16x16x32_bf16(ayh[kb], bh, acc[nt], 0, 0, 0);
+          acc[nt] = __builtin_amdgcn_mfma_f32_16x16x32_bf16(ayl[kb], bh, acc[nt], 0, 0, 0);
+          acc[nt] = __builtin_amdgcn_mfma_f32_16x16x32_bf16(ayh[kb], bl, acc[nt], 0, 0, 0);
+        }
+        if (kb < 3) {
+          int nxt = cur ^ 1;
+          BsC[nxt][0][w][l]     = r0;
+          BsC[nxt][0][w + 4][l] = r1;
+          BsC[nxt][1][w][l]     = r2;
+          BsC[nxt][1][w + 4][l] = r3;
+        }
+        __syncthreads();
+      }
+
+      int r0g = rbase + w * 16 + kg * 4;
+#pragma unroll
+      for (int nt = 0; nt < 8; ++nt) {
+        float bv = bo3[cbase + nt * 16 + ln];
+#pragma unroll
+        for (int j = 0; j < 4; ++j) {
+          out[(size_t)(r0g + j) * 256 + cbase + nt * 16 + ln] = acc[nt][j] + bv;
+        }
       }
     }
   }
@@ -663,25 +755,20 @@
   float* coef_glob = (float*)(al_glob + MAXACT * 128);
   __bf16* w2rt_h   = (__bf16*)(coef_glob + MAXACT * 192);
   __bf16* w2rt_l   = w2rt_h + 4608 * 128;
-  float* part      = (float*)(w2rt_l + 4608 * 128);
-  __bf16* xh       = (__bf16*)big;
-  __bf16* xl       = xh + (size_t)32768 * 128;
-
-  k_prep<<<103, 256, 0, stream>>>(w2_rad, wo2, wo3, abs_idx, h, wg1,
+  float* part2     = (float*)(w2rt_l + 4608 * 128);
+
+  k_prep<<<359, 256, 0, stream>>>(w2_rad, wo2, wo3, abs_idx, h, wg1,
+                                  e_feat, we1, be1, we2, be2,
                                   w2rt_h, w2rt_l, w2t_h, w2t_l, w3t_h, w3t_l,
-                                  habs_g, vabs, widx, count);
+                                  habs_g, vabs, widx, count, sfull);
   k_scatter<<<16, 256, 0, stream>>>(att_dst, widx);
   k_build<<<32, 256, 0, stream>>>(widx, active, count);
   k_node4<<<1024, 128, 0, stream>>>(count, active, widx, att_dist, att_vec, z, w_zemb,
                                     abs_idx, w1_rad, b1_rad, h, habs_g, wg1, bg1, wg2, bg2,
                                     h_full, ah_glob, al_glob, coef_glob, meta_f, meta_b);
-  k_mrgemm<<<dim3(36, 32), 256, 0, stream>>>(count, ah_glob, al_glob, w2rt_h, w2rt_l,
-                                             b2_rad, coef_glob, part);
-  k_post<<<2560, 256, 0, stream>>>(count, part, meta_f, meta_b, vabs,
-                                   e_feat, we1, be1, we2, be2, sfull);
-  k_hg1<<<512, 256, 0, stream>>>(vabs, sfull, wo1, bo1, xh, xl);
-  k_mgemm<0><<<dim3(1, 512), 256, 0, stream>>>(xh, xl, w2t_h, w2t_l, bo2,
-                                               xh, xl, nullptr);
-  k_mgemm<1><<<dim3(2, 512), 256, 0, stream>>>(xh, xl, w3t_h, w3t_l, bo3,
-                                               nullptr, nullptr, out);
-}
+  k_mrgemm2<<<dim3(12, 32), 256, 0, stream>>>(count, ah_glob, al_glob, w2rt_h, w2rt_l,
+                                              b2_rad, coef_glob, part2);
+  k_combine<<<2048, 256, 0, stream>>>(count, part2, meta_f, meta_b, vabs);
+  k_head<<<512, 256, 0, stream>>>(vabs, sfull, wo1, bo1, w2t_h, w2t_l, bo2,
+                                  w3t_h, w3t_l, bo3, out);
+}
```
